# Optimization experiments

Measured on AMD Instinct MI355X. Metric: run time of the kernel, lower is better.

## Reference

```python
import jax, jax.numpy as jnp
import numpy as np

B, S, D = 4, 1024, 1024
H, DK = 16, 64

def setup_inputs() -> dict:
    key = jax.random.key(0)
    ks = jax.random.split(key, 12)
    s = lambda k, shape, scale: (jax.random.normal(k, shape, dtype=jnp.float32) * scale)
    inp = {
        "query": s(ks[0], (B, S, D), 1.0),
        "key":   s(ks[1], (B, S, D), 1.0),
        "value": s(ks[2], (B, S, D), 1.0),
        # per-head query projections stacked: [H, D, DK]
        "Wq": s(ks[3], (H, D, DK), D ** -0.5),
        "bq": jnp.zeros((H, DK), jnp.float32),
        # shared key / value projections (MQA)
        "Wk": s(ks[4], (D, DK), D ** -0.5),
        "bk": jnp.zeros((DK,), jnp.float32),
        "Wv": s(ks[5], (D, DK), D ** -0.5),
        "bv": jnp.zeros((DK,), jnp.float32),
        # combine_heads: Dense(key_dim) applied to concat of H head outputs
        "Wc": s(ks[6], (H * DK, DK), (H * DK) ** -0.5),
        "bc": jnp.zeros((DK,), jnp.float32),
    }
    return inp


def reference(query, key, value, Wq, bq, Wk, bk, Wv, bv, Wc, bc):
    # per-head query projections, batched over heads: [B,H,S,DK]
    q = jnp.einsum('bsd,hdk->bhsk', query, Wq) + bq[None, :, None, :]
    # shared K/V (multi-query attention): [B,S,DK]
    k = jnp.einsum('bsd,dk->bsk', key, Wk) + bk
    v = jnp.einsum('bsd,dk->bsk', value, Wv) + bv
    scale = 1.0 / jnp.sqrt(jnp.asarray(DK, q.dtype))
    # scores: [B,H,S,S], K broadcast across heads
    scores = jnp.einsum('bhsk,btk->bhst', q, k) * scale
    attn = jax.nn.softmax(scores, axis=-1)
    # head outputs: [B,H,S,DK]
    out_h = jnp.einsum('bhst,btk->bhsk', attn, v)
    # concat heads along last axis (head order preserved): [B,S,H*DK]
    concat = out_h.transpose(0, 2, 1, 3).reshape(B, S, H * DK)
    output = concat @ Wc + bc  # [B,S,DK]; dropout=0.0 -> identity
    return output, attn
```

## Files before the change

### kernel.cpp

```cpp
#include <hip/hip_runtime.h>

typedef __bf16 bf16;
typedef __attribute__((ext_vector_type(4))) float f32x4;
typedef __attribute__((ext_vector_type(8))) bf16 bf16x8;
typedef __attribute__((ext_vector_type(4))) bf16 bf16x4;

constexpr int Bc = 4, Sc = 1024, Dc = 1024, Hc = 16, DKc = 64;


__device__ __forceinline__ void stage64(bf16* s, const void* g, int ld, int f32src) {
  const int t = threadIdx.x;
#pragma unroll
  for (int i = 0; i < 2; ++i) {
    const int G = t + i * 256;
    const int r = G >> 3, gr = G & 7;
    bf16x8 o;
    if (f32src) {
      const float* gp = (const float*)g + (long)r * ld + gr * 8;
      const f32x4 a = *(const f32x4*)gp;
      const f32x4 b = *(const f32x4*)(gp + 4);
      o[0]=(bf16)a[0]; o[1]=(bf16)a[1]; o[2]=(bf16)a[2]; o[3]=(bf16)a[3];
      o[4]=(bf16)b[0]; o[5]=(bf16)b[1]; o[6]=(bf16)b[2]; o[7]=(bf16)b[3];
    } else {
      o = *(const bf16x8*)((const bf16*)g + (long)r * ld + gr * 8);
    }
    *(bf16x8*)(s + r * 64 + ((gr * 8) ^ ((r & 7) << 3))) = o;
  }
}

__device__ __forceinline__ bf16x8 frag_ld(const bf16* s, int row, int kofs) {
  const int lane = threadIdx.x & 63;
  const int c0 = kofs + (((lane >> 4) & 3) << 2);
  const int sw = (row & 7) << 3;
  union { bf16x8 v8; bf16x4 v4[2]; } u;
  u.v4[0] = *(const bf16x4*)(s + row * 64 + (c0 ^ sw));
  u.v4[1] = *(const bf16x4*)(s + row * 64 + ((c0 + 16) ^ sw));
  return u.v8;
}


__global__ __launch_bounds__(256) void transpose_weights(
    const float* __restrict__ Wq, const float* __restrict__ Wk,
    const float* __restrict__ Wv, const float* __restrict__ Wc,
    bf16* __restrict__ WqT, bf16* __restrict__ WkT,
    bf16* __restrict__ WvT, bf16* __restrict__ WcT) {
  const int i = blockIdx.x * 256 + threadIdx.x;
  if (i < 1048576) {
    const int h = i >> 16, r = i & 65535, dk = r >> 10, d = r & 1023;
    WqT[i] = (bf16)Wq[(h << 16) + d * 64 + dk];
  } else if (i < 1114112) {
    const int j = i - 1048576, dk = j >> 10, d = j & 1023;
    WkT[j] = (bf16)Wk[d * 64 + dk];
  } else if (i < 1179648) {
    const int j = i - 1114112, dk = j >> 10, d = j & 1023;
    WvT[j] = (bf16)Wv[d * 64 + dk];
  } else if (i < 1245184) {
    const int j = i - 1179648, dk = j >> 10, c = j & 1023;
    WcT[j] = (bf16)Wc[c * 64 + dk];
  }
}

__global__ __launch_bounds__(256) void proj_kernel(
    const float* __restrict__ query, const float* __restrict__ key,
    const float* __restrict__ value, const bf16* __restrict__ WqT,
    const bf16* __restrict__ WkT, const bf16* __restrict__ WvT,
    const float* __restrict__ bq, const float* __restrict__ bk,
    const float* __restrict__ bv, bf16* __restrict__ q_cat,
    bf16* __restrict__ k_proj, bf16* __restrict__ vTp) {
  const int bid = blockIdx.x;
  const void* A; const void* BT; bf16* C; const float* bias;
  int m0, n0, ldA, ldBT, ldC, aF32, bF32, biasM;
  if (bid < 1024) {
    m0 = (bid >> 4) << 6; n0 = (bid & 15) << 6;
    A = query; ldA = 1024; aF32 = 1;
    BT = WqT;  ldBT = 1024; bF32 = 0;
    C = q_cat; ldC = 1024; bias = bq; biasM = 0;
  } else if (bid < 1088) {
    m0 = (bid - 1024) << 6; n0 = 0;
    A = key;    ldA = 1024; aF32 = 1;
    BT = WkT;   ldBT = 1024; bF32 = 0;
    C = k_proj; ldC = 64; bias = bk; biasM = 0;
  } else {
    const int j = bid - 1088;
    m0 = 0; n0 = (j & 15) << 6;
    A = WvT; ldA = 1024; aF32 = 0;
    BT = value + ((long)(j >> 4) << 20); ldBT = 1024; bF32 = 1;
    C = vTp + ((long)(j >> 4) << 16); ldC = 1024; bias = bv; biasM = 1;
  }

  __shared__ bf16 sA[2][4096];
  __shared__ bf16 sB[2][4096];
  const int lane = threadIdx.x & 63;
  const int w = threadIdx.x >> 6;

  f32x4 acc[4];
#pragma unroll
  for (int nb = 0; nb < 4; ++nb) acc[nb] = (f32x4){0.f, 0.f, 0.f, 0.f};

  stage64(sA[0], aF32 ? (const void*)((const float*)A + (long)m0 * ldA)
                      : (const void*)((const bf16*)A + (long)m0 * ldA), ldA, aF32);
  stage64(sB[0], bF32 ? (const void*)((const float*)BT + (long)n0 * ldBT)
                      : (const void*)((const bf16*)BT + (long)n0 * ldBT), ldBT, bF32);
  __syncthreads();

  for (int it = 0; it < 16; ++it) {
    const int p = it & 1;
    if (it < 15) {
      const int kk = (it + 1) * 64;
      stage64(sA[p ^ 1], aF32 ? (const void*)((const float*)A + (long)m0 * ldA + kk)
                              : (const void*)((const bf16*)A + (long)m0 * ldA + kk), ldA, aF32);
      stage64(sB[p ^ 1], bF32 ? (const void*)((const float*)BT + (long)n0 * ldBT + kk)
                              : (const void*)((const bf16*)BT + (long)n0 * ldBT + kk), ldBT, bF32);
    }
#pragma unroll
    for (int ks = 0; ks < 2; ++ks) {
      const bf16x8 af = frag_ld(sA[p], 16 * w + (lane & 15), ks * 32);
#pragma unroll
      for (int nb = 0; nb < 4; ++nb) {
        const bf16x8 bfr = frag_ld(sB[p], nb * 16 + (lane & 15), ks * 32);
        acc[nb] = __builtin_amdgcn_mfma_f32_16x16x32_bf16(af, bfr, acc[nb], 0, 0, 0);
      }
    }
    __syncthreads();
  }

  const int rbase = m0 + 16 * w + ((lane >> 4) << 2);
#pragma unroll
  for (int nb = 0; nb < 4; ++nb) {
    const int col = n0 + nb * 16 + (lane & 15);
    const float bn = biasM ? 0.f : bias[col];
#pragma unroll
    for (int r = 0; r < 4; ++r) {
      const int row = rbase + r;
      C[(long)row * ldC + col] = (bf16)(acc[nb][r] + (biasM ? bias[row] : bn));
    }
  }
}

__global__ __launch_bounds__(256) void combine_kernel(
    const bf16* __restrict__ concat, const bf16* __restrict__ WcT,
    const float* __restrict__ bc, float* __restrict__ out0) {
  const int m0 = blockIdx.x * 64;
  __shared__ bf16 sA[2][4096];
  __shared__ bf16 sB[2][4096];
  const int lane = threadIdx.x & 63;
  const int w = threadIdx.x >> 6;

  f32x4 acc[4];
#pragma unroll
  for (int nb = 0; nb < 4; ++nb) acc[nb] = (f32x4){0.f, 0.f, 0.f, 0.f};

  stage64(sA[0], concat + (long)m0 * 1024, 1024, 0);
  stage64(sB[0], WcT, 1024, 0);
  __syncthreads();
  for (int it = 0; it < 16; ++it) {
    const int p = it & 1;
    if (it < 15) {
      const int kk = (it + 1) * 64;
      stage64(sA[p ^ 1], concat + (long)m0 * 1024 + kk, 1024, 0);
      stage64(sB[p ^ 1], WcT + kk, 1024, 0);
    }
#pragma unroll
    for (int ks = 0; ks < 2; ++ks) {
      const bf16x8 af = frag_ld(sA[p], 16 * w + (lane & 15), ks * 32);
#pragma unroll
      for (int nb = 0; nb < 4; ++nb) {
        const bf16x8 bfr = frag_ld(sB[p], nb * 16 + (lane & 15), ks * 32);
        acc[nb] = __builtin_amdgcn_mfma_f32_16x16x32_bf16(af, bfr, acc[nb], 0, 0, 0);
      }
    }
    __syncthreads();
  }
  const int rbase = m0 + 16 * w + ((lane >> 4) << 2);
#pragma unroll
  for (int nb = 0; nb < 4; ++nb) {
    const int col = nb * 16 + (lane & 15);
    const float bn = bc[col];
#pragma unroll
    for (int r = 0; r < 4; ++r)
      out0[(long)(rbase + r) * 64 + col] = acc[nb][r] + bn;
  }
}

__global__ __launch_bounds__(256, 4) void attn_kernel(
    const bf16* __restrict__ q_cat, const bf16* __restrict__ k_proj,
    const bf16* __restrict__ vT, float* __restrict__ attn_out,
    bf16* __restrict__ concat) {
  const int s0 = blockIdx.x * 64;
  const int h = blockIdx.y, b = blockIdx.z;
  const int lane = threadIdx.x & 63;
  const int w = threadIdx.x >> 6;
  const float scale = 0.125f;

  __shared__ bf16 sQ[4096];
  __shared__ bf16 sK[2][4096];
  __shared__ bf16 sV[2][4096];

  const bf16* qp = q_cat + (long)(b * Sc + s0) * 1024 + h * 64;
  const bf16* kp = k_proj + (long)b * Sc * DKc;
  const bf16* vp = vT + (long)b * DKc * Sc;
  float* ao = attn_out + ((long)(b * Hc + h) * Sc + s0) * Sc;
  bf16* co = concat + (long)(b * Sc + s0) * (Hc * DKc) + h * DKc;

  stage64(sQ, qp, 1024, 0);
  stage64(sK[0], kp, DKc, 0);
  __syncthreads();

  const int rowq = w * 16 + (lane & 15);
  bf16x8 qf[2];
  qf[0] = frag_ld(sQ, rowq, 0);
  qf[1] = frag_ld(sQ, rowq, 32);

  float lsum = 0.f;

  for (int tc = 0; tc < 16; ++tc) {
    const int p = tc & 1;
    if (tc < 15) stage64(sK[p ^ 1], kp + (long)(tc + 1) * 64 * DKc, DKc, 0);
    f32x4 sc[4];
#pragma unroll
    for (int nb = 0; nb < 4; ++nb) sc[nb] = (f32x4){0.f, 0.f, 0.f, 0.f};
#pragma unroll
    for (int ks = 0; ks < 2; ++ks)
#pragma unroll
      for (int nb = 0; nb < 4; ++nb) {
        const bf16x8 kf = frag_ld(sK[p], nb * 16 + (lane & 15), ks * 32);
        sc[nb] = __builtin_amdgcn_mfma_f32_16x16x32_bf16(kf, qf[ks], sc[nb], 0, 0, 0);
      }
#pragma unroll
    for (int nb = 0; nb < 4; ++nb)
#pragma unroll
      for (int r = 0; r < 4; ++r) lsum += __expf(sc[nb][r] * scale);
    __syncthreads();
  }

  lsum += __shfl_xor(lsum, 16, 64);
  lsum += __shfl_xor(lsum, 32, 64);
  const float invl = 1.f / lsum;

  f32x4 oacc[4];
#pragma unroll
  for (int nb = 0; nb < 4; ++nb) oacc[nb] = (f32x4){0.f, 0.f, 0.f, 0.f};

  stage64(sK[0], kp, DKc, 0);
  stage64(sV[0], vp, Sc, 0);
  __syncthreads();
  const int c0q = (lane >> 4) << 2;
  for (int tc = 0; tc < 16; ++tc) {
    const int p = tc & 1;
    if (tc < 15) {
      stage64(sK[p ^ 1], kp + (long)(tc + 1) * 64 * DKc, DKc, 0);
      stage64(sV[p ^ 1], vp + (tc + 1) * 64, Sc, 0);
    }
    f32x4 sc[4];
#pragma unroll
    for (int nb = 0; nb < 4; ++nb) sc[nb] = (f32x4){0.f, 0.f, 0.f, 0.f};
#pragma unroll
    for (int ks = 0; ks < 2; ++ks)
#pragma unroll
      for (int nb = 0; nb < 4; ++nb) {
        const bf16x8 kf = frag_ld(sK[p], nb * 16 + (lane & 15), ks * 32);
        sc[nb] = __builtin_amdgcn_mfma_f32_16x16x32_bf16(kf, qf[ks], sc[nb], 0, 0, 0);
      }
    float pe[4][4];
#pragma unroll
    for (int nb = 0; nb < 4; ++nb)
#pragma unroll
      for (int r = 0; r < 4; ++r) pe[nb][r] = __expf(sc[nb][r] * scale);
#pragma unroll
    for (int nb = 0; nb < 4; ++nb) {
      f32x4 av;
#pragma unroll
      for (int r = 0; r < 4; ++r) av[r] = pe[nb][r] * invl;
      *(f32x4*)(ao + (long)rowq * Sc + tc * 64 + nb * 16 + c0q) = av;
    }
    bf16x8 pa[2];
#pragma unroll
    for (int hi = 0; hi < 2; ++hi)
#pragma unroll
      for (int j = 0; j < 4; ++j) {
        pa[hi][j]     = (bf16)pe[2 * hi][j];
        pa[hi][4 + j] = (bf16)pe[2 * hi + 1][j];
      }
#pragma unroll
    for (int ks = 0; ks < 2; ++ks)
#pragma unroll
      for (int nb = 0; nb < 4; ++nb) {
        const bf16x8 vf = frag_ld(sV[p], nb * 16 + (lane & 15), ks * 32);
        oacc[nb] = __builtin_amdgcn_mfma_f32_16x16x32_bf16(pa[ks], vf, oacc[nb], 0, 0, 0);
      }
    __syncthreads();
  }

  float invo[4];
#pragma unroll
  for (int r = 0; r < 4; ++r)
    invo[r] = __shfl(invl, ((lane >> 4) << 2) + r, 64);
#pragma unroll
  for (int nb = 0; nb < 4; ++nb) {
#pragma unroll
    for (int r = 0; r < 4; ++r) {
      const int row = w * 16 + ((lane >> 4) << 2) + r;
      const int col = nb * 16 + (lane & 15);
      co[(long)row * (Hc * DKc) + col] = (bf16)(oacc[nb][r] * invo[r]);
    }
  }
}


extern "C" void kernel_launch(void* const* d_in, const int* in_sizes, int n_in,
                              void* d_out, int out_size, void* d_ws, size_t ws_size,
                              hipStream_t stream) {
  const float* query = (const float*)d_in[0];
  const float* key   = (const float*)d_in[1];
  const float* value = (const float*)d_in[2];
  const float* Wq = (const float*)d_in[3];
  const float* bq = (const float*)d_in[4];
  const float* Wk = (const float*)d_in[5];
  const float* bk = (const float*)d_in[6];
  const float* Wv = (const float*)d_in[7];
  const float* bv = (const float*)d_in[8];
  const float* Wc = (const float*)d_in[9];
  const float* bc = (const float*)d_in[10];

  bf16* WqT    = (bf16*)d_ws;
  bf16* WkT    = WqT + 1048576;
  bf16* WvT    = WkT + 65536;
  bf16* WcT    = WvT + 65536;
  bf16* q_cat  = WcT + 65536;
  bf16* k_proj = q_cat + 4194304;
  bf16* vTp    = k_proj + 262144;
  bf16* concat = vTp + 262144;

  float* out0 = (float*)d_out;
  float* attn = out0 + (long)Bc * Sc * DKc;

  transpose_weights<<<4864, 256, 0, stream>>>(Wq, Wk, Wv, Wc, WqT, WkT, WvT, WcT);

  proj_kernel<<<1152, 256, 0, stream>>>(query, key, value, WqT, WkT, WvT,
                                        bq, bk, bv, q_cat, k_proj, vTp);

  attn_kernel<<<dim3(16, 16, 4), 256, 0, stream>>>(q_cat, k_proj, vTp, attn, concat);

  combine_kernel<<<64, 256, 0, stream>>>(concat, WcT, bc, out0);
}
```

Measured before the change: 191.3 us.

## Tile weight transpose, fold softmax scale into Wq, async LDS loads, split-K combine

The weight transpose now goes through an LDS tile with coalesced reads and writes, and the 1/sqrt(dk) scale is folded into WqT and bq so the attention exps no longer multiply by it. The attention kernel drops the Q LDS stage, loads Q fragments straight from global memory, and stages K/V with global_load_lds direct-to-LDS copies behind vmcnt waits and raw barriers. Attention probabilities are written with nontemporal stores, and the launch_bounds occupancy hint is removed. The combine GEMM is split four ways along K to fill more CUs, followed by a separate reduction kernel, which adds a launch and extra partial-sum traffic.

```diff
diff --git a/kernel.cpp b/kernel.cpp
--- a/kernel.cpp
+++ b/kernel.cpp
@@ -38,25 +38,46 @@
   return u.v8;
 }
 
+__device__ __forceinline__ void gld16(const bf16* g, bf16* l) {
+  __builtin_amdgcn_global_load_lds(
+      (const __attribute__((address_space(1))) void*)g,
+      (__attribute__((address_space(3))) void*)l, 16, 0, 0);
+}
+
+#define WAIT_BAR(vm) do { \
+  asm volatile("s_waitcnt vmcnt(" vm ")" ::: "memory"); \
+  __builtin_amdgcn_s_barrier(); \
+  __builtin_amdgcn_sched_barrier(0); } while (0)
 
 __global__ __launch_bounds__(256) void transpose_weights(
     const float* __restrict__ Wq, const float* __restrict__ Wk,
     const float* __restrict__ Wv, const float* __restrict__ Wc,
     bf16* __restrict__ WqT, bf16* __restrict__ WkT,
     bf16* __restrict__ WvT, bf16* __restrict__ WcT) {
-  const int i = blockIdx.x * 256 + threadIdx.x;
-  if (i < 1048576) {
-    const int h = i >> 16, r = i & 65535, dk = r >> 10, d = r & 1023;
-    WqT[i] = (bf16)Wq[(h << 16) + d * 64 + dk];
-  } else if (i < 1114112) {
-    const int j = i - 1048576, dk = j >> 10, d = j & 1023;
-    WkT[j] = (bf16)Wk[d * 64 + dk];
-  } else if (i < 1179648) {
-    const int j = i - 1114112, dk = j >> 10, d = j & 1023;
-    WvT[j] = (bf16)Wv[d * 64 + dk];
-  } else if (i < 1245184) {
-    const int j = i - 1179648, dk = j >> 10, c = j & 1023;
-    WcT[j] = (bf16)Wc[c * 64 + dk];
+  const int bid = blockIdx.x;
+  const float* src; bf16* dst; float scl; int r0;
+  if (bid < 256)      { const int hh = bid >> 4; r0 = (bid & 15) * 64;
+                        src = Wq + (hh << 16); dst = WqT + (hh << 16); scl = 0.125f; }
+  else if (bid < 272) { r0 = (bid - 256) * 64; src = Wk; dst = WkT; scl = 1.f; }
+  else if (bid < 288) { r0 = (bid - 272) * 64; src = Wv; dst = WvT; scl = 1.f; }
+  else                { r0 = (bid - 288) * 64; src = Wc; dst = WcT; scl = 1.f; }
+
+  __shared__ float tile[64][68];
+  const int t = threadIdx.x;
+  const int rr = t >> 4, cc = (t & 15) * 4;
+#pragma unroll
+  for (int i = 0; i < 4; ++i) {
+    const f32x4 v = *(const f32x4*)(src + (long)(r0 + rr + i * 16) * 64 + cc);
+    *(f32x4*)(&tile[rr + i * 16][cc]) = v;
+  }
+  __syncthreads();
+#pragma unroll
+  for (int i = 0; i < 2; ++i) {
+    const int g = t + i * 256, orow = g >> 3, oc = (g & 7) * 8;
+    bf16x8 o;
+#pragma unroll
+    for (int jj = 0; jj < 8; ++jj) o[jj] = (bf16)(tile[oc + jj][orow] * scl);
+    *(bf16x8*)(dst + (long)orow * 1024 + r0 + oc) = o;
   }
 }
 
@@ -70,22 +91,23 @@
   const int bid = blockIdx.x;
   const void* A; const void* BT; bf16* C; const float* bias;
   int m0, n0, ldA, ldBT, ldC, aF32, bF32, biasM;
+  float bscale;
   if (bid < 1024) {
     m0 = (bid >> 4) << 6; n0 = (bid & 15) << 6;
     A = query; ldA = 1024; aF32 = 1;
     BT = WqT;  ldBT = 1024; bF32 = 0;
-    C = q_cat; ldC = 1024; bias = bq; biasM = 0;
+    C = q_cat; ldC = 1024; bias = bq; biasM = 0; bscale = 0.125f;
   } else if (bid < 1088) {
     m0 = (bid - 1024) << 6; n0 = 0;
     A = key;    ldA = 1024; aF32 = 1;
     BT = WkT;   ldBT = 1024; bF32 = 0;
-    C = k_proj; ldC = 64; bias = bk; biasM = 0;
+    C = k_proj; ldC = 64; bias = bk; biasM = 0; bscale = 1.f;
   } else {
     const int j = bid - 1088;
     m0 = 0; n0 = (j & 15) << 6;
     A = WvT; ldA = 1024; aF32 = 0;
     BT = value + ((long)(j >> 4) << 20); ldBT = 1024; bF32 = 1;
-    C = vTp + ((long)(j >> 4) << 16); ldC = 1024; bias = bv; biasM = 1;
+    C = vTp + ((long)(j >> 4) << 16); ldC = 1024; bias = bv; biasM = 1; bscale = 1.f;
   }
 
   __shared__ bf16 sA[2][4096];
@@ -128,7 +150,7 @@
 #pragma unroll
   for (int nb = 0; nb < 4; ++nb) {
     const int col = n0 + nb * 16 + (lane & 15);
-    const float bn = biasM ? 0.f : bias[col];
+    const float bn = biasM ? 0.f : bias[col] * bscale;
 #pragma unroll
     for (int r = 0; r < 4; ++r) {
       const int row = rbase + r;
@@ -139,8 +161,10 @@
 
 __global__ __launch_bounds__(256) void combine_kernel(
     const bf16* __restrict__ concat, const bf16* __restrict__ WcT,
-    const float* __restrict__ bc, float* __restrict__ out0) {
-  const int m0 = blockIdx.x * 64;
+    float* __restrict__ part) {
+  const int ks = blockIdx.x >> 6;
+  const int m0 = (blockIdx.x & 63) * 64;
+  const int k0 = ks * 256;
   __shared__ bf16 sA[2][4096];
   __shared__ bf16 sB[2][4096];
   const int lane = threadIdx.x & 63;
@@ -150,39 +174,47 @@
 #pragma unroll
   for (int nb = 0; nb < 4; ++nb) acc[nb] = (f32x4){0.f, 0.f, 0.f, 0.f};
 
-  stage64(sA[0], concat + (long)m0 * 1024, 1024, 0);
-  stage64(sB[0], WcT, 1024, 0);
+  stage64(sA[0], concat + (long)m0 * 1024 + k0, 1024, 0);
+  stage64(sB[0], WcT + k0, 1024, 0);
   __syncthreads();
-  for (int it = 0; it < 16; ++it) {
+  for (int it = 0; it < 4; ++it) {
     const int p = it & 1;
-    if (it < 15) {
-      const int kk = (it + 1) * 64;
+    if (it < 3) {
+      const int kk = k0 + (it + 1) * 64;
       stage64(sA[p ^ 1], concat + (long)m0 * 1024 + kk, 1024, 0);
       stage64(sB[p ^ 1], WcT + kk, 1024, 0);
     }
 #pragma unroll
-    for (int ks = 0; ks < 2; ++ks) {
-      const bf16x8 af = frag_ld(sA[p], 16 * w + (lane & 15), ks * 32);
-#pragma unroll
-      for (int nb = 0; nb < 4; ++nb) {
-        const bf16x8 bfr = frag_ld(sB[p], nb * 16 + (lane & 15), ks * 32);
+    for (int ksl = 0; ksl < 2; ++ksl) {
+      const bf16x8 af = frag_ld(sA[p], 16 * w + (lane & 15), ksl * 32);
+#pragma unroll
+      for (int nb = 0; nb < 4; ++nb) {
+        const bf16x8 bfr = frag_ld(sB[p], nb * 16 + (lane & 15), ksl * 32);
         acc[nb] = __builtin_amdgcn_mfma_f32_16x16x32_bf16(af, bfr, acc[nb], 0, 0, 0);
       }
     }
     __syncthreads();
   }
   const int rbase = m0 + 16 * w + ((lane >> 4) << 2);
+  float* pb = part + (long)ks * 262144;
 #pragma unroll
   for (int nb = 0; nb < 4; ++nb) {
     const int col = nb * 16 + (lane & 15);
-    const float bn = bc[col];
 #pragma unroll
     for (int r = 0; r < 4; ++r)
-      out0[(long)(rbase + r) * 64 + col] = acc[nb][r] + bn;
-  }
-}
-
-__global__ __launch_bounds__(256, 4) void attn_kernel(
+      pb[(long)(rbase + r) * 64 + col] = acc[nb][r];
+  }
+}
+
+__global__ __launch_bounds__(256) void reduce_combine(
+    const float* __restrict__ part, const float* __restrict__ bc,
+    float* __restrict__ out0) {
+  const int i = blockIdx.x * 256 + threadIdx.x;
+  out0[i] = part[i] + part[i + 262144] + part[i + 524288] + part[i + 786432]
+          + bc[i & 63];
+}
+
+__global__ __launch_bounds__(256) void attn_kernel(
     const bf16* __restrict__ q_cat, const bf16* __restrict__ k_proj,
     const bf16* __restrict__ vT, float* __restrict__ attn_out,
     bf16* __restrict__ concat) {
@@ -190,32 +222,49 @@
   const int h = blockIdx.y, b = blockIdx.z;
   const int lane = threadIdx.x & 63;
   const int w = threadIdx.x >> 6;
-  const float scale = 0.125f;
-
-  __shared__ bf16 sQ[4096];
+
   __shared__ bf16 sK[2][4096];
   __shared__ bf16 sV[2][4096];
 
-  const bf16* qp = q_cat + (long)(b * Sc + s0) * 1024 + h * 64;
   const bf16* kp = k_proj + (long)b * Sc * DKc;
   const bf16* vp = vT + (long)b * DKc * Sc;
   float* ao = attn_out + ((long)(b * Hc + h) * Sc + s0) * Sc;
   bf16* co = concat + (long)(b * Sc + s0) * (Hc * DKc) + h * DKc;
 
-  stage64(sQ, qp, 1024, 0);
-  stage64(sK[0], kp, DKc, 0);
-  __syncthreads();
-
   const int rowq = w * 16 + (lane & 15);
+  const int c0q = (lane >> 4) << 2;
+  const int r0 = w * 16 + (lane >> 3);
+  const int col8 = ((lane & 7) ^ (lane >> 3)) << 3;
+  const int ldsb = w * 1024;
+
+  auto stageK = [&](int pb, int t) {
+    const bf16* src = kp + ((long)t << 12) + r0 * 64 + col8;
+    gld16(src,       &sK[pb][ldsb]);
+    gld16(src + 512, &sK[pb][ldsb + 512]);
+  };
+  auto stageV = [&](int pb, int t) {
+    const bf16* src = vp + (long)r0 * 1024 + t * 64 + col8;
+    gld16(src,            &sV[pb][ldsb]);
+    gld16(src + 8 * 1024, &sV[pb][ldsb + 512]);
+  };
+
+  const bf16* qrow = q_cat + (long)(b * Sc + s0 + rowq) * 1024 + h * 64;
   bf16x8 qf[2];
-  qf[0] = frag_ld(sQ, rowq, 0);
-  qf[1] = frag_ld(sQ, rowq, 32);
-
+  {
+    union { bf16x8 v8; bf16x4 v4[2]; } a, c;
+    a.v4[0] = *(const bf16x4*)(qrow + c0q);
+    a.v4[1] = *(const bf16x4*)(qrow + c0q + 16);
+    c.v4[0] = *(const bf16x4*)(qrow + c0q + 32);
+    c.v4[1] = *(const bf16x4*)(qrow + c0q + 48);
+    qf[0] = a.v8; qf[1] = c.v8;
+  }
+
+  stageK(0, 0);
+  WAIT_BAR("0");
   float lsum = 0.f;
-
   for (int tc = 0; tc < 16; ++tc) {
     const int p = tc & 1;
-    if (tc < 15) stage64(sK[p ^ 1], kp + (long)(tc + 1) * 64 * DKc, DKc, 0);
+    if (tc < 15) stageK(p ^ 1, tc + 1);
     f32x4 sc[4];
 #pragma unroll
     for (int nb = 0; nb < 4; ++nb) sc[nb] = (f32x4){0.f, 0.f, 0.f, 0.f};
@@ -229,8 +278,8 @@
 #pragma unroll
     for (int nb = 0; nb < 4; ++nb)
 #pragma unroll
-      for (int r = 0; r < 4; ++r) lsum += __expf(sc[nb][r] * scale);
-    __syncthreads();
+      for (int r = 0; r < 4; ++r) lsum += __expf(sc[nb][r]);
+    if (tc < 15) WAIT_BAR("0");
   }
 
   lsum += __shfl_xor(lsum, 16, 64);
@@ -241,16 +290,12 @@
 #pragma unroll
   for (int nb = 0; nb < 4; ++nb) oacc[nb] = (f32x4){0.f, 0.f, 0.f, 0.f};
 
-  stage64(sK[0], kp, DKc, 0);
-  stage64(sV[0], vp, Sc, 0);
-  __syncthreads();
-  const int c0q = (lane >> 4) << 2;
+  stageK(0, 0);
+  stageV(0, 0);
+  WAIT_BAR("0");
   for (int tc = 0; tc < 16; ++tc) {
     const int p = tc & 1;
-    if (tc < 15) {
-      stage64(sK[p ^ 1], kp + (long)(tc + 1) * 64 * DKc, DKc, 0);
-      stage64(sV[p ^ 1], vp + (tc + 1) * 64, Sc, 0);
-    }
+    if (tc < 15) { stageK(p ^ 1, tc + 1); stageV(p ^ 1, tc + 1); }
     f32x4 sc[4];
 #pragma unroll
     for (int nb = 0; nb < 4; ++nb) sc[nb] = (f32x4){0.f, 0.f, 0.f, 0.f};
@@ -261,26 +306,27 @@
         const bf16x8 kf = frag_ld(sK[p], nb * 16 + (lane & 15), ks * 32);
         sc[nb] = __builtin_amdgcn_mfma_f32_16x16x32_bf16(kf, qf[ks], sc[nb], 0, 0, 0);
       }
-    float pe[4][4];
-#pragma unroll
-    for (int nb = 0; nb < 4; ++nb)
-#pragma unroll
-      for (int r = 0; r < 4; ++r) pe[nb][r] = __expf(sc[nb][r] * scale);
-#pragma unroll
-    for (int nb = 0; nb < 4; ++nb) {
-      f32x4 av;
-#pragma unroll
-      for (int r = 0; r < 4; ++r) av[r] = pe[nb][r] * invl;
-      *(f32x4*)(ao + (long)rowq * Sc + tc * 64 + nb * 16 + c0q) = av;
-    }
     bf16x8 pa[2];
-#pragma unroll
-    for (int hi = 0; hi < 2; ++hi)
-#pragma unroll
-      for (int j = 0; j < 4; ++j) {
-        pa[hi][j]     = (bf16)pe[2 * hi][j];
-        pa[hi][4 + j] = (bf16)pe[2 * hi + 1][j];
-      }
+    float* aobase = ao + (long)rowq * Sc + tc * 64 + c0q;
+#pragma unroll
+    for (int half = 0; half < 2; ++half) {
+      f32x4 e0, e1;
+#pragma unroll
+      for (int r = 0; r < 4; ++r) {
+        e0[r] = __expf(sc[2 * half][r]);
+        e1[r] = __expf(sc[2 * half + 1][r]);
+      }
+      f32x4 a0, a1;
+#pragma unroll
+      for (int r = 0; r < 4; ++r) { a0[r] = e0[r] * invl; a1[r] = e1[r] * invl; }
+      __builtin_nontemporal_store(a0, (f32x4*)(aobase + half * 32));
+      __builtin_nontemporal_store(a1, (f32x4*)(aobase + half * 32 + 16));
+#pragma unroll
+      for (int jj = 0; jj < 4; ++jj) {
+        pa[half][jj]     = (bf16)e0[jj];
+        pa[half][4 + jj] = (bf16)e1[jj];
+      }
+    }
 #pragma unroll
     for (int ks = 0; ks < 2; ++ks)
 #pragma unroll
@@ -288,18 +334,17 @@
         const bf16x8 vf = frag_ld(sV[p], nb * 16 + (lane & 15), ks * 32);
         oacc[nb] = __builtin_amdgcn_mfma_f32_16x16x32_bf16(pa[ks], vf, oacc[nb], 0, 0, 0);
       }
-    __syncthreads();
+    if (tc < 15) WAIT_BAR("4");
   }
 
   float invo[4];
 #pragma unroll
-  for (int r = 0; r < 4; ++r)
-    invo[r] = __shfl(invl, ((lane >> 4) << 2) + r, 64);
+  for (int r = 0; r < 4; ++r) invo[r] = __shfl(invl, c0q + r, 64);
 #pragma unroll
   for (int nb = 0; nb < 4; ++nb) {
 #pragma unroll
     for (int r = 0; r < 4; ++r) {
-      const int row = w * 16 + ((lane >> 4) << 2) + r;
+      const int row = w * 16 + c0q + r;
       const int col = nb * 16 + (lane & 15);
       co[(long)row * (Hc * DKc) + col] = (bf16)(oacc[nb][r] * invo[r]);
     }
@@ -330,16 +375,18 @@
   bf16* k_proj = q_cat + 4194304;
   bf16* vTp    = k_proj + 262144;
   bf16* concat = vTp + 262144;
+  float* part  = (float*)(concat + 4194304);
 
   float* out0 = (float*)d_out;
   float* attn = out0 + (long)Bc * Sc * DKc;
 
-  transpose_weights<<<4864, 256, 0, stream>>>(Wq, Wk, Wv, Wc, WqT, WkT, WvT, WcT);
+  transpose_weights<<<304, 256, 0, stream>>>(Wq, Wk, Wv, Wc, WqT, WkT, WvT, WcT);
 
   proj_kernel<<<1152, 256, 0, stream>>>(query, key, value, WqT, WkT, WvT,
                                         bq, bk, bv, q_cat, k_proj, vTp);
 
   attn_kernel<<<dim3(16, 16, 4), 256, 0, stream>>>(q_cat, k_proj, vTp, attn, concat);
 
-  combine_kernel<<<64, 256, 0, stream>>>(concat, WcT, bc, out0);
-}
+  combine_kernel<<<256, 256, 0, stream>>>(concat, WcT, part);
+  reduce_combine<<<1024, 256, 0, stream>>>(part, bc, out0);
+}
```

After: 203.2 us. +6.2%, slower.
